# Optimization experiments

Hardware: AMD Instinct MI355X
Metric: run time of the kernel (lower is better)

The kernel has to match this reference:

```python
import jax, jax.numpy as jnp
import numpy as np

B, IN, V, H, OUT = 4096, 1024, 48, 512, 64

def setup_inputs() -> dict:
    key = jax.random.key(0)
    ks = jax.random.split(key, 6)
    s = 0.02
    x = jax.random.normal(ks[0], (B, IN), dtype=jnp.float32)
    # stacked per-vocab MLP params: hidden layers have bias, last layer bias=False
    W1 = jax.random.normal(ks[1], (V, IN, H), dtype=jnp.float32) * s
    b1 = jax.random.normal(ks[2], (V, H), dtype=jnp.float32) * s
    W2 = jax.random.normal(ks[3], (V, H, H), dtype=jnp.float32) * s
    b2 = jax.random.normal(ks[4], (V, H), dtype=jnp.float32) * s
    W3 = jax.random.normal(ks[5], (V, H, OUT), dtype=jnp.float32) * s
    return {"x": x, "W1": W1, "b1": b1, "W2": W2, "b2": b2, "W3": W3}

def reference(x, W1, b1, W2, b2, W3):
    # grouped GEMM over the vocab axis; equivalent to the per-MLP loop + cat
    h = jax.nn.relu(jnp.einsum('bi,vih->bvh', x, W1) + b1)      # [B, V, H]
    h = jax.nn.relu(jnp.einsum('bvh,vhk->bvk', h, W2) + b2)     # [B, V, H]
    o = jnp.einsum('bvk,vko->bvo', h, W3)                        # [B, V, OUT]
    # torch.cat([...], dim=-1) == reshape since outputs are in vocab order
    return o.reshape(x.shape[0], V * OUT)
```

## Files before the change

### kernel.cpp

```cpp
#include <hip/hip_runtime.h>

#define B_SZ   4096
#define IN_SZ  1024
#define V_SZ   48
#define H_SZ   512
#define OUT_SZ 64

typedef __attribute__((ext_vector_type(4))) float f32x4;
typedef __attribute__((ext_vector_type(8))) short bf16x8;
typedef __attribute__((ext_vector_type(4))) short short4v;
typedef __attribute__((ext_vector_type(4))) float float4v;

__device__ __forceinline__ short f2bf(float f){
    unsigned u = __builtin_bit_cast(unsigned, f);
    u += 0x7fffu + ((u >> 16) & 1u);
    return (short)(u >> 16);
}

__device__ __forceinline__ void gl2lds16(const void* g, void* l){
    __builtin_amdgcn_global_load_lds(
        (const __attribute__((address_space(1))) void*)g,
        (__attribute__((address_space(3))) void*)l, 16, 0, 0);
}

__global__ void k_convert_x(const float* __restrict__ x, short* __restrict__ xb){
    int i = blockIdx.x * 256 + threadIdx.x;
    float4v f = ((const float4v*)x)[i];
    short4v o = { f2bf(f.x), f2bf(f.y), f2bf(f.z), f2bf(f.w) };
    ((short4v*)xb)[i] = o;
}

__global__ __launch_bounds__(256) void k_transpose_cvt4(
    const float* __restrict__ in, short* __restrict__ out, int R, int C)
{
    __shared__ short t[64][68];
    int v  = blockIdx.z;
    int c0 = blockIdx.x * 64, r0 = blockIdx.y * 64;
    int tid = threadIdx.x;
    size_t base = (size_t)v * R * C;
    const float* inp = in + base + (size_t)r0 * C + c0;
    int g    = tid >> 4;
    int col4 = (tid & 15) * 4;
    #pragma unroll
    for (int p = 0; p < 4; ++p){
        int row = p*16 + g;
        float4v f = *(const float4v*)&inp[(size_t)row * C + col4];
        short4v s = { f2bf(f.x), f2bf(f.y), f2bf(f.z), f2bf(f.w) };
        *(short4v*)&t[row][col4] = s;
    }
    __syncthreads();
    short* outp = out + base + (size_t)c0 * R + r0;
    int r4 = (tid & 15) * 4;
    #pragma unroll
    for (int p = 0; p < 4; ++p){
        int c = p*16 + g;
        short4v s = { t[r4+0][c], t[r4+1][c], t[r4+2][c], t[r4+3][c] };
        *(short4v*)&outp[(size_t)c * R + r4] = s;
    }
}

__global__ __launch_bounds__(256) void k_gemm1(
    const short* __restrict__ xb, const short* __restrict__ W1t,
    const float* __restrict__ b1, short* __restrict__ h1)
{
    __shared__ __align__(16) short As[128*64];
    __shared__ __align__(16) short Bs[128*64];
    const int tid  = threadIdx.x;
    const int lane = tid & 63, wave = tid >> 6;
    const int l15  = lane & 15, quad = lane >> 4;
    const int wm = wave & 1, wn = wave >> 1;
    const int M0 = blockIdx.x * 128;
    const int N0 = blockIdx.y * 128;
    const int v  = blockIdx.z;

    const short* a_base = xb  + (size_t)M0 * IN_SZ;
    const short* b_base = W1t + ((size_t)v * H_SZ + N0) * IN_SZ;

    const short* asrc[4]; const short* bsrc[4]; short* adst[4]; short* bdst[4];
    #pragma unroll
    for (int j = 0; j < 4; ++j){
        int p   = j*256 + tid;
        int row = p >> 3;
        int w   = (p & 7) ^ (row & 7);
        asrc[j] = a_base + (size_t)row * IN_SZ + w*8;
        bsrc[j] = b_base + (size_t)row * IN_SZ + w*8;
        adst[j] = &As[(size_t)(j*256 + (tid & ~63)) * 8];
        bdst[j] = &Bs[(size_t)(j*256 + (tid & ~63)) * 8];
    }

    f32x4 acc[4][4];
    #pragma unroll
    for (int i = 0; i < 4; ++i)
        #pragma unroll
        for (int j = 0; j < 4; ++j) acc[i][j] = (f32x4){0.f,0.f,0.f,0.f};

    for (int k0 = 0; k0 < IN_SZ; k0 += 64){
        #pragma unroll
        for (int j = 0; j < 4; ++j){
            gl2lds16(asrc[j] + k0, adst[j]);
            gl2lds16(bsrc[j] + k0, bdst[j]);
        }
        __syncthreads();
        #pragma unroll
        for (int kk = 0; kk < 2; ++kk){
            bf16x8 a[4], b[4];
            #pragma unroll
            for (int tm = 0; tm < 4; ++tm){
                int m = wm*64 + tm*16 + l15;
                int slot = m*8 + ((kk*4 + quad) ^ (m & 7));
                a[tm] = *(const bf16x8*)&As[slot*8];
            }
            #pragma unroll
            for (int tn = 0; tn < 4; ++tn){
                int n = wn*64 + tn*16 + l15;
                int slot = n*8 + ((kk*4 + quad) ^ (n & 7));
                b[tn] = *(const bf16x8*)&Bs[slot*8];
            }
            #pragma unroll
            for (int tm = 0; tm < 4; ++tm)
                #pragma unroll
                for (int tn = 0; tn < 4; ++tn)
                    acc[tm][tn] = __builtin_amdgcn_mfma_f32_16x16x32_bf16(
                        a[tm], b[tn], acc[tm][tn], 0, 0, 0);
        }
        __syncthreads();
    }

    const float* bv = b1 + (size_t)v * H_SZ;
    short* cv = h1 + (size_t)v * (B_SZ*H_SZ);
    #pragma unroll
    for (int tn = 0; tn < 4; ++tn){
        int col = N0 + wn*64 + tn*16 + l15;
        float bb = bv[col];
        #pragma unroll
        for (int tm = 0; tm < 4; ++tm){
            int rowb = M0 + wm*64 + tm*16 + quad*4;
            #pragma unroll
            for (int r = 0; r < 4; ++r){
                float val = acc[tm][tn][r] + bb;
                val = val > 0.f ? val : 0.f;
                cv[(size_t)(rowb + r) * H_SZ + col] = f2bf(val);
            }
        }
    }
}

__global__ __launch_bounds__(512) void k_gemm23(
    const short* __restrict__ h, const short* __restrict__ W2t,
    const float* __restrict__ b2, const short* __restrict__ W3t,
    float* __restrict__ out)
{
    __shared__ __align__(16) short As[64*64];
    __shared__ __align__(16) short Bs[512*64];
    const int tid  = threadIdx.x;
    const int lane = tid & 63, wave = tid >> 6;
    const int l15  = lane & 15, quad = lane >> 4;
    const int M0 = blockIdx.x * 64;
    const int v  = blockIdx.y;

    const short* hv  = h   + (size_t)v * (B_SZ*H_SZ) + (size_t)M0 * H_SZ;
    const short* w2v = W2t + (size_t)v * (H_SZ*H_SZ);
    const short* w3v = W3t + (size_t)v * (OUT_SZ*H_SZ);

    const int rowT = tid >> 3;
    const int wT   = (tid & 7) ^ (rowT & 7);
    const short* asrc  = hv  + (size_t)rowT * H_SZ + wT*8;
    const short* bsrc0 = w2v + (size_t)rowT * H_SZ + wT*8;
    short* adst  = &As[(size_t)(tid & ~63) * 8];
    short* bdst0 = &Bs[(size_t)(tid & ~63) * 8];

    f32x4 acc[4][4];
    #pragma unroll
    for (int i = 0; i < 4; ++i)
        #pragma unroll
        for (int j = 0; j < 4; ++j) acc[i][j] = (f32x4){0.f,0.f,0.f,0.f};

    for (int k0 = 0; k0 < H_SZ; k0 += 64){
        gl2lds16(asrc + k0, adst);
        #pragma unroll
        for (int j = 0; j < 8; ++j)
            gl2lds16(bsrc0 + (size_t)j*(64*H_SZ) + k0, bdst0 + (size_t)j*512*8);
        __syncthreads();
        #pragma unroll
        for (int kk = 0; kk < 2; ++kk){
            bf16x8 a[4], b[4];
            #pragma unroll
            for (int tm = 0; tm < 4; ++tm){
                int m = tm*16 + l15;
                int slot = m*8 + ((kk*4 + quad) ^ (m & 7));
                a[tm] = *(const bf16x8*)&As[slot*8];
            }
            #pragma unroll
            for (int tn = 0; tn < 4; ++tn){
                int n = wave*64 + tn*16 + l15;
                int slot = n*8 + ((kk*4 + quad) ^ (n & 7));
                b[tn] = *(const bf16x8*)&Bs[slot*8];
            }
            #pragma unroll
            for (int tm = 0; tm < 4; ++tm)
                #pragma unroll
                for (int tn = 0; tn < 4; ++tn)
                    acc[tm][tn] = __builtin_amdgcn_mfma_f32_16x16x32_bf16(
                        a[tm], b[tn], acc[tm][tn], 0, 0, 0);
        }
        __syncthreads();
    }

    const float* bv = b2 + (size_t)v * H_SZ;
    #pragma unroll
    for (int tn = 0; tn < 4; ++tn){
        int col = wave*64 + tn*16 + l15;
        float bb = bv[col];
        int u = col >> 3, c7 = col & 7;
        #pragma unroll
        for (int tm = 0; tm < 4; ++tm){
            int rowb = tm*16 + quad*4;
            #pragma unroll
            for (int r = 0; r < 4; ++r){
                int row = rowb + r;
                float val = acc[tm][tn][r] + bb;
                val = val > 0.f ? val : 0.f;
                Bs[row*512 + ((u ^ (row & 7))*8) + c7] = f2bf(val);
            }
        }
    }
    __syncthreads();

    if (wave < 4){
        f32x4 acc3[4];
        #pragma unroll
        for (int i = 0; i < 4; ++i) acc3[i] = (f32x4){0.f,0.f,0.f,0.f};
        const int n3 = wave*16 + l15;
        const short* b3p = &w3v[(size_t)n3 * H_SZ + quad*8];
        #pragma unroll
        for (int kk = 0; kk < 16; ++kk){
            bf16x8 bfrag = *(const bf16x8*)&b3p[kk*32];
            int u = kk*4 + quad;
            #pragma unroll
            for (int tm = 0; tm < 4; ++tm){
                int m = tm*16 + l15;
                bf16x8 afrag = *(const bf16x8*)&Bs[m*512 + ((u ^ (m & 7))*8)];
                acc3[tm] = __builtin_amdgcn_mfma_f32_16x16x32_bf16(
                    afrag, bfrag, acc3[tm], 0, 0, 0);
            }
        }
        const int col = v*OUT_SZ + wave*16 + l15;
        #pragma unroll
        for (int tm = 0; tm < 4; ++tm){
            int rowb = M0 + tm*16 + quad*4;
            #pragma unroll
            for (int r = 0; r < 4; ++r)
                out[(size_t)(rowb + r) * (V_SZ*OUT_SZ) + col] = acc3[tm][r];
        }
    }
}

extern "C" void kernel_launch(void* const* d_in, const int* in_sizes, int n_in,
                              void* d_out, int out_size, void* d_ws, size_t ws_size,
                              hipStream_t stream)
{
    (void)in_sizes; (void)n_in; (void)out_size; (void)ws_size;
    const float* x  = (const float*)d_in[0];
    const float* W1 = (const float*)d_in[1];
    const float* b1 = (const float*)d_in[2];
    const float* W2 = (const float*)d_in[3];
    const float* b2 = (const float*)d_in[4];
    const float* W3 = (const float*)d_in[5];
    float* out = (float*)d_out;

    char* ws = (char*)d_ws;
    short* xb  = (short*)ws;  ws += (size_t)B_SZ * IN_SZ * 2;
    short* W1t = (short*)ws;  ws += (size_t)V_SZ * H_SZ * IN_SZ * 2;
    short* W2t = (short*)ws;  ws += (size_t)V_SZ * H_SZ * H_SZ * 2;
    short* W3t = (short*)ws;  ws += (size_t)V_SZ * OUT_SZ * H_SZ * 2;
    short* h1  = (short*)ws;

    k_convert_x<<<dim3(B_SZ*IN_SZ/1024), dim3(256), 0, stream>>>(x, xb);
    k_transpose_cvt4<<<dim3(H_SZ/64,  IN_SZ/64, V_SZ), dim3(256), 0, stream>>>(W1, W1t, IN_SZ, H_SZ);
    k_transpose_cvt4<<<dim3(H_SZ/64,  H_SZ/64,  V_SZ), dim3(256), 0, stream>>>(W2, W2t, H_SZ, H_SZ);
    k_transpose_cvt4<<<dim3(OUT_SZ/64,H_SZ/64,  V_SZ), dim3(256), 0, stream>>>(W3, W3t, H_SZ, OUT_SZ);

    k_gemm1 <<<dim3(B_SZ/128, H_SZ/128, V_SZ), dim3(256), 0, stream>>>(xb, W1t, b1, h1);
    k_gemm23<<<dim3(B_SZ/64, V_SZ), dim3(512), 0, stream>>>(h1, W2t, b2, W3t, out);
}
```

Before: 653.1 us.

## Rewrite gemm1 as 256x256 double-buffered pipelined tile with 8 waves

The first grouped GEMM moves to 256x256 output tiles per 512-thread block, with double-buffered LDS and async global-to-LDS prefetch of the next A and B tiles interleaved with MFMA phases. It adds explicit barriers, vmcnt waits and s_setprio around the MFMA bursts. The aim is to hide load latency and raise arithmetic intensity per byte loaded. In exchange it uses more registers and 128KB of LDS per block, and the hand-tuned waitcnt counts leave little margin for ordering mistakes.

```diff
diff --git a/kernel.cpp b/kernel.cpp
--- a/kernel.cpp
+++ b/kernel.cpp
@@ -22,6 +22,8 @@
         (const __attribute__((address_space(1))) void*)g,
         (__attribute__((address_space(3))) void*)l, 16, 0, 0);
 }
+
+#define MFMA_B16(d, a, b) d = __builtin_amdgcn_mfma_f32_16x16x32_bf16(a, b, d, 0, 0, 0)
 
 __global__ void k_convert_x(const float* __restrict__ x, short* __restrict__ xb){
     int i = blockIdx.x * 256 + threadIdx.x;
@@ -59,85 +61,142 @@
     }
 }
 
-__global__ __launch_bounds__(256) void k_gemm1(
+#define G1_TILE (256*64)
+#define G1_NT   (IN_SZ/64)
+
+__global__ __launch_bounds__(512) void k_gemm1(
     const short* __restrict__ xb, const short* __restrict__ W1t,
     const float* __restrict__ b1, short* __restrict__ h1)
 {
-    __shared__ __align__(16) short As[128*64];
-    __shared__ __align__(16) short Bs[128*64];
+    __shared__ __align__(16) short As[2*G1_TILE];
+    __shared__ __align__(16) short Bs[2*G1_TILE];
     const int tid  = threadIdx.x;
     const int lane = tid & 63, wave = tid >> 6;
     const int l15  = lane & 15, quad = lane >> 4;
-    const int wm = wave & 1, wn = wave >> 1;
-    const int M0 = blockIdx.x * 128;
-    const int N0 = blockIdx.y * 128;
+    const int wm = wave >> 2, wn = wave & 3;
+    const int M0 = blockIdx.x * 256;
+    const int N0 = blockIdx.y * 256;
     const int v  = blockIdx.z;
 
-    const short* a_base = xb  + (size_t)M0 * IN_SZ;
-    const short* b_base = W1t + ((size_t)v * H_SZ + N0) * IN_SZ;
-
-    const short* asrc[4]; const short* bsrc[4]; short* adst[4]; short* bdst[4];
-    #pragma unroll
-    for (int j = 0; j < 4; ++j){
-        int p   = j*256 + tid;
-        int row = p >> 3;
-        int w   = (p & 7) ^ (row & 7);
-        asrc[j] = a_base + (size_t)row * IN_SZ + w*8;
-        bsrc[j] = b_base + (size_t)row * IN_SZ + w*8;
-        adst[j] = &As[(size_t)(j*256 + (tid & ~63)) * 8];
-        bdst[j] = &Bs[(size_t)(j*256 + (tid & ~63)) * 8];
-    }
-
-    f32x4 acc[4][4];
-    #pragma unroll
-    for (int i = 0; i < 4; ++i)
+    const short* apan = xb  + (size_t)M0 * IN_SZ;
+    const short* bpan = W1t + ((size_t)v * H_SZ + N0) * IN_SZ;
+
+    const int lr    = tid >> 3;
+    const int toff  = lr * IN_SZ + (((tid & 7) ^ (lr & 7)) * 8);
+    const int wbase = tid & ~63;
+
+    auto stage = [&](const short* pan, short* lbase, int h, int j, int t){
+        gl2lds16(pan + (size_t)(h*128 + j*64) * IN_SZ + t*64 + toff,
+                 lbase + (h*1024 + j*512 + wbase) * 8);
+    };
+    auto stage_half = [&](const short* pan, short* lbase, int h, int t){
+        stage(pan, lbase, h, 0, t);
+        stage(pan, lbase, h, 1, t);
+    };
+
+    stage_half(apan, As, 0, 0); stage_half(apan, As, 1, 0);
+    stage_half(bpan, Bs, 0, 0); stage_half(bpan, Bs, 1, 0);
+    stage_half(apan, As + G1_TILE, 0, 1); stage_half(apan, As + G1_TILE, 1, 1);
+    asm volatile("s_waitcnt vmcnt(4)" ::: "memory");
+    __builtin_amdgcn_s_barrier();
+
+    f32x4 acc[8][4];
+    #pragma unroll
+    for (int i = 0; i < 8; ++i)
         #pragma unroll
         for (int j = 0; j < 4; ++j) acc[i][j] = (f32x4){0.f,0.f,0.f,0.f};
 
-    for (int k0 = 0; k0 < IN_SZ; k0 += 64){
-        #pragma unroll
-        for (int j = 0; j < 4; ++j){
-            gl2lds16(asrc[j] + k0, adst[j]);
-            gl2lds16(bsrc[j] + k0, bdst[j]);
-        }
-        __syncthreads();
-        #pragma unroll
-        for (int kk = 0; kk < 2; ++kk){
-            bf16x8 a[4], b[4];
-            #pragma unroll
-            for (int tm = 0; tm < 4; ++tm){
-                int m = wm*64 + tm*16 + l15;
-                int slot = m*8 + ((kk*4 + quad) ^ (m & 7));
-                a[tm] = *(const bf16x8*)&As[slot*8];
-            }
-            #pragma unroll
-            for (int tn = 0; tn < 4; ++tn){
-                int n = wn*64 + tn*16 + l15;
-                int slot = n*8 + ((kk*4 + quad) ^ (n & 7));
-                b[tn] = *(const bf16x8*)&Bs[slot*8];
-            }
-            #pragma unroll
-            for (int tm = 0; tm < 4; ++tm)
-                #pragma unroll
-                for (int tn = 0; tn < 4; ++tn)
-                    acc[tm][tn] = __builtin_amdgcn_mfma_f32_16x16x32_bf16(
-                        a[tm], b[tn], acc[tm][tn], 0, 0, 0);
-        }
-        __syncthreads();
+    const int x7 = l15 & 7;
+    const int abase = (wm*128 + l15) * 64;
+    const int bbase = (wn*64  + l15) * 64;
+    const int c_kk0 = ((quad)     ^ x7) * 8;
+    const int c_kk1 = ((quad + 4) ^ x7) * 8;
+
+    #pragma unroll 2
+    for (int t = 0; t < G1_NT; ++t){
+        short* Ac = As + (t & 1) * G1_TILE;
+        short* Bc = Bs + (t & 1) * G1_TILE;
+        short* Bn = Bs + ((t + 1) & 1) * G1_TILE;
+
+        bf16x8 a0[8], a1[8];
+
+        #pragma unroll
+        for (int rf = 0; rf < 8; ++rf)
+            a0[rf] = *(const bf16x8*)&Ac[abase + rf*1024 + c_kk0];
+        bf16x8 b00 = *(const bf16x8*)&Bc[bbase + 0*1024 + c_kk0];
+        bf16x8 b01 = *(const bf16x8*)&Bc[bbase + 1*1024 + c_kk0];
+        if (t + 1 < G1_NT) stage_half(bpan, Bn, 0, t + 1);
+        __builtin_amdgcn_s_barrier();
+        asm volatile("s_waitcnt lgkmcnt(0)" ::: "memory");
+        __builtin_amdgcn_s_setprio(1);
+        #pragma unroll
+        for (int rf = 0; rf < 8; ++rf){
+            MFMA_B16(acc[rf][0], a0[rf], b00);
+            MFMA_B16(acc[rf][1], a0[rf], b01);
+        }
+        __builtin_amdgcn_s_setprio(0);
+        __builtin_amdgcn_s_barrier();
+
+        #pragma unroll
+        for (int rf = 0; rf < 8; ++rf)
+            a1[rf] = *(const bf16x8*)&Ac[abase + rf*1024 + c_kk1];
+        bf16x8 b02 = *(const bf16x8*)&Bc[bbase + 2*1024 + c_kk0];
+        bf16x8 b03 = *(const bf16x8*)&Bc[bbase + 3*1024 + c_kk0];
+        if (t + 1 < G1_NT) stage_half(bpan, Bn, 1, t + 1);
+        __builtin_amdgcn_s_barrier();
+        asm volatile("s_waitcnt lgkmcnt(0)" ::: "memory");
+        __builtin_amdgcn_s_setprio(1);
+        #pragma unroll
+        for (int rf = 0; rf < 8; ++rf){
+            MFMA_B16(acc[rf][2], a0[rf], b02);
+            MFMA_B16(acc[rf][3], a0[rf], b03);
+        }
+        __builtin_amdgcn_s_setprio(0);
+        __builtin_amdgcn_s_barrier();
+
+        bf16x8 b10 = *(const bf16x8*)&Bc[bbase + 0*1024 + c_kk1];
+        bf16x8 b11 = *(const bf16x8*)&Bc[bbase + 1*1024 + c_kk1];
+        if (t + 2 < G1_NT) stage_half(apan, Ac, 0, t + 2);
+        __builtin_amdgcn_s_barrier();
+        asm volatile("s_waitcnt lgkmcnt(0)" ::: "memory");
+        __builtin_amdgcn_s_setprio(1);
+        #pragma unroll
+        for (int rf = 0; rf < 8; ++rf){
+            MFMA_B16(acc[rf][0], a1[rf], b10);
+            MFMA_B16(acc[rf][1], a1[rf], b11);
+        }
+        __builtin_amdgcn_s_setprio(0);
+        __builtin_amdgcn_s_barrier();
+
+        bf16x8 b12 = *(const bf16x8*)&Bc[bbase + 2*1024 + c_kk1];
+        bf16x8 b13 = *(const bf16x8*)&Bc[bbase + 3*1024 + c_kk1];
+        if (t + 2 < G1_NT) stage_half(apan, Ac, 1, t + 2);
+        __builtin_amdgcn_s_barrier();
+        asm volatile("s_waitcnt lgkmcnt(0)" ::: "memory");
+        __builtin_amdgcn_s_setprio(1);
+        #pragma unroll
+        for (int rf = 0; rf < 8; ++rf){
+            MFMA_B16(acc[rf][2], a1[rf], b12);
+            MFMA_B16(acc[rf][3], a1[rf], b13);
+        }
+        __builtin_amdgcn_s_setprio(0);
+        if (t + 2 < G1_NT)      { asm volatile("s_waitcnt vmcnt(4)" ::: "memory"); }
+        else if (t + 1 < G1_NT) { asm volatile("s_waitcnt vmcnt(0)" ::: "memory"); }
+        __builtin_amdgcn_s_barrier();
     }
 
     const float* bv = b1 + (size_t)v * H_SZ;
     short* cv = h1 + (size_t)v * (B_SZ*H_SZ);
     #pragma unroll
-    for (int tn = 0; tn < 4; ++tn){
-        int col = N0 + wn*64 + tn*16 + l15;
+    for (int cf = 0; cf < 4; ++cf){
+        int col = N0 + wn*64 + cf*16 + l15;
         float bb = bv[col];
         #pragma unroll
-        for (int tm = 0; tm < 4; ++tm){
-            int rowb = M0 + wm*64 + tm*16 + quad*4;
+        for (int rf = 0; rf < 8; ++rf){
+            int rowb = M0 + wm*128 + rf*16 + quad*4;
             #pragma unroll
             for (int r = 0; r < 4; ++r){
-                float val = acc[tm][tn][r] + bb;
+                float val = acc[rf][cf][r] + bb;
                 val = val > 0.f ? val : 0.f;
                 cv[(size_t)(rowb + r) * H_SZ + col] = f2bf(val);
             }
@@ -280,6 +339,6 @@
     k_transpose_cvt4<<<dim3(H_SZ/64,  H_SZ/64,  V_SZ), dim3(256), 0, stream>>>(W2, W2t, H_SZ, H_SZ);
     k_transpose_cvt4<<<dim3(OUT_SZ/64,H_SZ/64,  V_SZ), dim3(256), 0, stream>>>(W3, W3t, H_SZ, OUT_SZ);
 
-    k_gemm1 <<<dim3(B_SZ/128, H_SZ/128, V_SZ), dim3(256), 0, stream>>>(xb, W1t, b1, h1);
+    k_gemm1 <<<dim3(B_SZ/256, H_SZ/256, V_SZ), dim3(512), 0, stream>>>(xb, W1t, b1, h1);
     k_gemm23<<<dim3(B_SZ/64, V_SZ), dim3(512), 0, stream>>>(h1, W2t, b2, W3t, out);
 }
```

After: 655.8 us. Within noise of the previous version (+0.4%).

## Read W2 fragments directly from global, double-buffer A tile, split GEMM3 across all waves

Applied to the files above, without the earlier changes.

k_gemm23 no longer stages the 512x64 W2 tile in LDS each k-step. Each wave now loads its W2 B-fragments straight from global/L2 into registers. The h activation tile is double-buffered in LDS so the next tile's load overlaps the current tile's MFMAs, with setprio raised around the MFMA block. The third GEMM is spread across all 8 waves (2x4 split) instead of 4, and launch bounds request 4 blocks per CU. This trims the W2 LDS traffic and syncs, but adds uncoalesced, L2-dependent global loads on the critical path.

```diff
diff --git a/kernel.cpp b/kernel.cpp
--- a/kernel.cpp
+++ b/kernel.cpp
@@ -22,6 +22,8 @@
         (const __attribute__((address_space(1))) void*)g,
         (__attribute__((address_space(3))) void*)l, 16, 0, 0);
 }
+
+#define MFMA_B16(d, a, b) d = __builtin_amdgcn_mfma_f32_16x16x32_bf16(a, b, d, 0, 0, 0)
 
 __global__ void k_convert_x(const float* __restrict__ x, short* __restrict__ xb){
     int i = blockIdx.x * 256 + threadIdx.x;
@@ -145,13 +147,15 @@
     }
 }
 
-__global__ __launch_bounds__(512) void k_gemm23(
+__global__ __launch_bounds__(512, 4) void k_gemm23(
     const short* __restrict__ h, const short* __restrict__ W2t,
     const float* __restrict__ b2, const short* __restrict__ W3t,
     float* __restrict__ out)
 {
-    __shared__ __align__(16) short As[64*64];
-    __shared__ __align__(16) short Bs[512*64];
+    __shared__ __align__(16) short smem[2*64*64 + 64*512];
+    short* As0 = smem;
+    short* As1 = smem + 4096;
+    short* h2s = smem + 8192;
     const int tid  = threadIdx.x;
     const int lane = tid & 63, wave = tid >> 6;
     const int l15  = lane & 15, quad = lane >> 4;
@@ -164,10 +168,10 @@
 
     const int rowT = tid >> 3;
     const int wT   = (tid & 7) ^ (rowT & 7);
-    const short* asrc  = hv  + (size_t)rowT * H_SZ + wT*8;
-    const short* bsrc0 = w2v + (size_t)rowT * H_SZ + wT*8;
-    short* adst  = &As[(size_t)(tid & ~63) * 8];
-    short* bdst0 = &Bs[(size_t)(tid & ~63) * 8];
+    const short* asrc = hv + (size_t)rowT * H_SZ + wT*8;
+    const int   aoff  = (tid & ~63) * 8;
+
+    const short* b2base = w2v + (size_t)(wave*64 + l15) * H_SZ + quad*8;
 
     f32x4 acc[4][4];
     #pragma unroll
@@ -175,82 +179,91 @@
         #pragma unroll
         for (int j = 0; j < 4; ++j) acc[i][j] = (f32x4){0.f,0.f,0.f,0.f};
 
-    for (int k0 = 0; k0 < H_SZ; k0 += 64){
-        gl2lds16(asrc + k0, adst);
-        #pragma unroll
-        for (int j = 0; j < 8; ++j)
-            gl2lds16(bsrc0 + (size_t)j*(64*H_SZ) + k0, bdst0 + (size_t)j*512*8);
-        __syncthreads();
+    auto cstep = [&](const short* Acur, int t){
         #pragma unroll
         for (int kk = 0; kk < 2; ++kk){
-            bf16x8 a[4], b[4];
-            #pragma unroll
-            for (int tm = 0; tm < 4; ++tm){
-                int m = tm*16 + l15;
+            bf16x8 b[4];
+            #pragma unroll
+            for (int nf = 0; nf < 4; ++nf)
+                b[nf] = *(const bf16x8*)&b2base[nf*(16*H_SZ) + t*64 + kk*32];
+            bf16x8 a[4];
+            #pragma unroll
+            for (int mf = 0; mf < 4; ++mf){
+                int m = mf*16 + l15;
                 int slot = m*8 + ((kk*4 + quad) ^ (m & 7));
-                a[tm] = *(const bf16x8*)&As[slot*8];
-            }
-            #pragma unroll
-            for (int tn = 0; tn < 4; ++tn){
-                int n = wave*64 + tn*16 + l15;
-                int slot = n*8 + ((kk*4 + quad) ^ (n & 7));
-                b[tn] = *(const bf16x8*)&Bs[slot*8];
-            }
-            #pragma unroll
-            for (int tm = 0; tm < 4; ++tm)
+                a[mf] = *(const bf16x8*)&Acur[slot*8];
+            }
+            __builtin_amdgcn_s_setprio(1);
+            #pragma unroll
+            for (int mf = 0; mf < 4; ++mf)
                 #pragma unroll
-                for (int tn = 0; tn < 4; ++tn)
-                    acc[tm][tn] = __builtin_amdgcn_mfma_f32_16x16x32_bf16(
-                        a[tm], b[tn], acc[tm][tn], 0, 0, 0);
-        }
+                for (int nf = 0; nf < 4; ++nf)
+                    MFMA_B16(acc[mf][nf], a[mf], b[nf]);
+            __builtin_amdgcn_s_setprio(0);
+        }
+    };
+
+    gl2lds16(asrc, As0 + aoff);
+    __syncthreads();
+
+    #pragma unroll
+    for (int tp = 0; tp < 4; ++tp){
+        int t = tp*2;
+        if (t + 1 < 8) gl2lds16(asrc + (t+1)*64, As1 + aoff);
+        cstep(As0, t);
+        __syncthreads();
+        if (t + 2 < 8) gl2lds16(asrc + (t+2)*64, As0 + aoff);
+        cstep(As1, t + 1);
         __syncthreads();
     }
 
     const float* bv = b2 + (size_t)v * H_SZ;
     #pragma unroll
-    for (int tn = 0; tn < 4; ++tn){
-        int col = wave*64 + tn*16 + l15;
+    for (int nf = 0; nf < 4; ++nf){
+        int col = wave*64 + nf*16 + l15;
         float bb = bv[col];
         int u = col >> 3, c7 = col & 7;
         #pragma unroll
-        for (int tm = 0; tm < 4; ++tm){
-            int rowb = tm*16 + quad*4;
+        for (int mf = 0; mf < 4; ++mf){
+            int rowb = mf*16 + quad*4;
             #pragma unroll
             for (int r = 0; r < 4; ++r){
                 int row = rowb + r;
-                float val = acc[tm][tn][r] + bb;
+                float val = acc[mf][nf][r] + bb;
                 val = val > 0.f ? val : 0.f;
-                Bs[row*512 + ((u ^ (row & 7))*8) + c7] = f2bf(val);
+                h2s[row*512 + ((u ^ (row & 7))*8) + c7] = f2bf(val);
             }
         }
     }
     __syncthreads();
 
-    if (wave < 4){
-        f32x4 acc3[4];
-        #pragma unroll
-        for (int i = 0; i < 4; ++i) acc3[i] = (f32x4){0.f,0.f,0.f,0.f};
-        const int n3 = wave*16 + l15;
+    {
+        const int wm3 = wave >> 2;
+        const int wn3 = wave & 3;
+        f32x4 acc3[2];
+        #pragma unroll
+        for (int i = 0; i < 2; ++i) acc3[i] = (f32x4){0.f,0.f,0.f,0.f};
+        const int n3 = wn3*16 + l15;
         const short* b3p = &w3v[(size_t)n3 * H_SZ + quad*8];
         #pragma unroll
         for (int kk = 0; kk < 16; ++kk){
             bf16x8 bfrag = *(const bf16x8*)&b3p[kk*32];
             int u = kk*4 + quad;
             #pragma unroll
-            for (int tm = 0; tm < 4; ++tm){
-                int m = tm*16 + l15;
-                bf16x8 afrag = *(const bf16x8*)&Bs[m*512 + ((u ^ (m & 7))*8)];
-                acc3[tm] = __builtin_amdgcn_mfma_f32_16x16x32_bf16(
-                    afrag, bfrag, acc3[tm], 0, 0, 0);
-            }
-        }
-        const int col = v*OUT_SZ + wave*16 + l15;
-        #pragma unroll
-        for (int tm = 0; tm < 4; ++tm){
-            int rowb = M0 + tm*16 + quad*4;
+            for (int mf = 0; mf < 2; ++mf){
+                int m = wm3*32 + mf*16 + l15;
+                bf16x8 afrag = *(const bf16x8*)&h2s[m*512 + ((u ^ (m & 7))*8)];
+                acc3[mf] = __builtin_amdgcn_mfma_f32_16x16x32_bf16(
+                    afrag, bfrag, acc3[mf], 0, 0, 0);
+            }
+        }
+        const int col = v*OUT_SZ + wn3*16 + l15;
+        #pragma unroll
+        for (int mf = 0; mf < 2; ++mf){
+            int rowb = M0 + wm3*32 + mf*16 + quad*4;
             #pragma unroll
             for (int r = 0; r < 4; ++r)
-                out[(size_t)(rowb + r) * (V_SZ*OUT_SZ) + col] = acc3[tm][r];
+                out[(size_t)(rowb + r) * (V_SZ*OUT_SZ) + col] = acc3[mf][r];
         }
     }
 }
```

Result: slower. 739.7 us (+13.3%).

## Split fused layer-2/3 kernel into separate tiled GEMMs with intermediate buffer

Applied to the files above, without the earlier changes.

Adds standalone k_gemm2 (128x128 tiles, bias+ReLU, bf16 output to a new h2 workspace) and k_gemm3 (128x64 tiles writing the final output). These replace the fused k_gemm23 when the workspace is large enough. The fused kernel used a 64-row tile with a 64KB LDS weight buffer, which likely limits occupancy and reuse. The split uses smaller LDS footprints and the same swizzled layout as gemm1, but costs an extra full write and read of the [V,B,H] intermediate, plus one more launch. It falls back to the fused kernel if the workspace is too small.

```diff
diff --git a/kernel.cpp b/kernel.cpp
--- a/kernel.cpp
+++ b/kernel.cpp
@@ -145,6 +145,177 @@
     }
 }
 
+__global__ __launch_bounds__(256) void k_gemm2(
+    const short* __restrict__ h1, const short* __restrict__ W2t,
+    const float* __restrict__ b2, short* __restrict__ h2)
+{
+    __shared__ __align__(16) short As[128*64];
+    __shared__ __align__(16) short Bs[128*64];
+    const int tid  = threadIdx.x;
+    const int lane = tid & 63, wave = tid >> 6;
+    const int l15  = lane & 15, quad = lane >> 4;
+    const int wm = wave & 1, wn = wave >> 1;
+    const int M0 = blockIdx.x * 128;
+    const int N0 = blockIdx.y * 128;
+    const int v  = blockIdx.z;
+
+    const short* a_base = h1  + (size_t)v * (B_SZ*H_SZ) + (size_t)M0 * H_SZ;
+    const short* b_base = W2t + ((size_t)v * H_SZ + N0) * H_SZ;
+
+    const short* asrc[4]; const short* bsrc[4]; short* adst[4]; short* bdst[4];
+    #pragma unroll
+    for (int j = 0; j < 4; ++j){
+        int p   = j*256 + tid;
+        int row = p >> 3;
+        int w   = (p & 7) ^ (row & 7);
+        asrc[j] = a_base + (size_t)row * H_SZ + w*8;
+        bsrc[j] = b_base + (size_t)row * H_SZ + w*8;
+        adst[j] = &As[(size_t)(j*256 + (tid & ~63)) * 8];
+        bdst[j] = &Bs[(size_t)(j*256 + (tid & ~63)) * 8];
+    }
+
+    f32x4 acc[4][4];
+    #pragma unroll
+    for (int i = 0; i < 4; ++i)
+        #pragma unroll
+        for (int j = 0; j < 4; ++j) acc[i][j] = (f32x4){0.f,0.f,0.f,0.f};
+
+    for (int k0 = 0; k0 < H_SZ; k0 += 64){
+        #pragma unroll
+        for (int j = 0; j < 4; ++j){
+            gl2lds16(asrc[j] + k0, adst[j]);
+            gl2lds16(bsrc[j] + k0, bdst[j]);
+        }
+        __syncthreads();
+        #pragma unroll
+        for (int kk = 0; kk < 2; ++kk){
+            bf16x8 a[4], b[4];
+            #pragma unroll
+            for (int tm = 0; tm < 4; ++tm){
+                int m = wm*64 + tm*16 + l15;
+                int slot = m*8 + ((kk*4 + quad) ^ (m & 7));
+                a[tm] = *(const bf16x8*)&As[slot*8];
+            }
+            #pragma unroll
+            for (int tn = 0; tn < 4; ++tn){
+                int n = wn*64 + tn*16 + l15;
+                int slot = n*8 + ((kk*4 + quad) ^ (n & 7));
+                b[tn] = *(const bf16x8*)&Bs[slot*8];
+            }
+            #pragma unroll
+            for (int tm = 0; tm < 4; ++tm)
+                #pragma unroll
+                for (int tn = 0; tn < 4; ++tn)
+                    acc[tm][tn] = __builtin_amdgcn_mfma_f32_16x16x32_bf16(
+                        a[tm], b[tn], acc[tm][tn], 0, 0, 0);
+        }
+        __syncthreads();
+    }
+
+    const float* bv = b2 + (size_t)v * H_SZ;
+    short* cv = h2 + (size_t)v * (B_SZ*H_SZ);
+    #pragma unroll
+    for (int tn = 0; tn < 4; ++tn){
+        int col = N0 + wn*64 + tn*16 + l15;
+        float bb = bv[col];
+        #pragma unroll
+        for (int tm = 0; tm < 4; ++tm){
+            int rowb = M0 + wm*64 + tm*16 + quad*4;
+            #pragma unroll
+            for (int r = 0; r < 4; ++r){
+                float val = acc[tm][tn][r] + bb;
+                val = val > 0.f ? val : 0.f;
+                cv[(size_t)(rowb + r) * H_SZ + col] = f2bf(val);
+            }
+        }
+    }
+}
+
+__global__ __launch_bounds__(256) void k_gemm3(
+    const short* __restrict__ h2, const short* __restrict__ W3t,
+    float* __restrict__ out)
+{
+    __shared__ __align__(16) short As[128*64];
+    __shared__ __align__(16) short Bs[64*64];
+    const int tid  = threadIdx.x;
+    const int lane = tid & 63, wave = tid >> 6;
+    const int l15  = lane & 15, quad = lane >> 4;
+    const int wm = wave & 1, wn = wave >> 1;
+    const int M0 = blockIdx.x * 128;
+    const int v  = blockIdx.z;
+
+    const short* a_base = h2  + (size_t)v * (B_SZ*H_SZ) + (size_t)M0 * H_SZ;
+    const short* b_base = W3t + (size_t)v * (OUT_SZ*H_SZ);
+
+    const short* asrc[4]; short* adst[4];
+    #pragma unroll
+    for (int j = 0; j < 4; ++j){
+        int p   = j*256 + tid;
+        int row = p >> 3;
+        int w   = (p & 7) ^ (row & 7);
+        asrc[j] = a_base + (size_t)row * H_SZ + w*8;
+        adst[j] = &As[(size_t)(j*256 + (tid & ~63)) * 8];
+    }
+    const short* bsrc[2]; short* bdst[2];
+    #pragma unroll
+    for (int j = 0; j < 2; ++j){
+        int p   = j*256 + tid;
+        int row = p >> 3;
+        int w   = (p & 7) ^ (row & 7);
+        bsrc[j] = b_base + (size_t)row * H_SZ + w*8;
+        bdst[j] = &Bs[(size_t)(j*256 + (tid & ~63)) * 8];
+    }
+
+    f32x4 acc[4][2];
+    #pragma unroll
+    for (int i = 0; i < 4; ++i)
+        #pragma unroll
+        for (int j = 0; j < 2; ++j) acc[i][j] = (f32x4){0.f,0.f,0.f,0.f};
+
+    for (int k0 = 0; k0 < H_SZ; k0 += 64){
+        #pragma unroll
+        for (int j = 0; j < 4; ++j) gl2lds16(asrc[j] + k0, adst[j]);
+        #pragma unroll
+        for (int j = 0; j < 2; ++j) gl2lds16(bsrc[j] + k0, bdst[j]);
+        __syncthreads();
+        #pragma unroll
+        for (int kk = 0; kk < 2; ++kk){
+            bf16x8 a[4], b[2];
+            #pragma unroll
+            for (int tm = 0; tm < 4; ++tm){
+                int m = wm*64 + tm*16 + l15;
+                int slot = m*8 + ((kk*4 + quad) ^ (m & 7));
+                a[tm] = *(const bf16x8*)&As[slot*8];
+            }
+            #pragma unroll
+            for (int tn = 0; tn < 2; ++tn){
+                int n = wn*32 + tn*16 + l15;
+                int slot = n*8 + ((kk*4 + quad) ^ (n & 7));
+                b[tn] = *(const bf16x8*)&Bs[slot*8];
+            }
+            #pragma unroll
+            for (int tm = 0; tm < 4; ++tm)
+                #pragma unroll
+                for (int tn = 0; tn < 2; ++tn)
+                    acc[tm][tn] = __builtin_amdgcn_mfma_f32_16x16x32_bf16(
+                        a[tm], b[tn], acc[tm][tn], 0, 0, 0);
+        }
+        __syncthreads();
+    }
+
+    #pragma unroll
+    for (int tn = 0; tn < 2; ++tn){
+        int col = v*OUT_SZ + wn*32 + tn*16 + l15;
+        #pragma unroll
+        for (int tm = 0; tm < 4; ++tm){
+            int rowb = M0 + wm*64 + tm*16 + quad*4;
+            #pragma unroll
+            for (int r = 0; r < 4; ++r)
+                out[(size_t)(rowb + r) * (V_SZ*OUT_SZ) + col] = acc[tm][tn][r];
+        }
+    }
+}
+
 __global__ __launch_bounds__(512) void k_gemm23(
     const short* __restrict__ h, const short* __restrict__ W2t,
     const float* __restrict__ b2, const short* __restrict__ W3t,
@@ -259,7 +430,7 @@
                               void* d_out, int out_size, void* d_ws, size_t ws_size,
                               hipStream_t stream)
 {
-    (void)in_sizes; (void)n_in; (void)out_size; (void)ws_size;
+    (void)in_sizes; (void)n_in; (void)out_size;
     const float* x  = (const float*)d_in[0];
     const float* W1 = (const float*)d_in[1];
     const float* b1 = (const float*)d_in[2];
@@ -273,13 +444,21 @@
     short* W1t = (short*)ws;  ws += (size_t)V_SZ * H_SZ * IN_SZ * 2;
     short* W2t = (short*)ws;  ws += (size_t)V_SZ * H_SZ * H_SZ * 2;
     short* W3t = (short*)ws;  ws += (size_t)V_SZ * OUT_SZ * H_SZ * 2;
-    short* h1  = (short*)ws;
+    short* h1  = (short*)ws;  ws += (size_t)V_SZ * B_SZ * H_SZ * 2;
+    short* h2  = (short*)ws;  ws += (size_t)V_SZ * B_SZ * H_SZ * 2;
+    const size_t need_split = (size_t)(ws - (char*)d_ws);
 
     k_convert_x<<<dim3(B_SZ*IN_SZ/1024), dim3(256), 0, stream>>>(x, xb);
     k_transpose_cvt4<<<dim3(H_SZ/64,  IN_SZ/64, V_SZ), dim3(256), 0, stream>>>(W1, W1t, IN_SZ, H_SZ);
     k_transpose_cvt4<<<dim3(H_SZ/64,  H_SZ/64,  V_SZ), dim3(256), 0, stream>>>(W2, W2t, H_SZ, H_SZ);
     k_transpose_cvt4<<<dim3(OUT_SZ/64,H_SZ/64,  V_SZ), dim3(256), 0, stream>>>(W3, W3t, H_SZ, OUT_SZ);
 
-    k_gemm1 <<<dim3(B_SZ/128, H_SZ/128, V_SZ), dim3(256), 0, stream>>>(xb, W1t, b1, h1);
-    k_gemm23<<<dim3(B_SZ/64, V_SZ), dim3(512), 0, stream>>>(h1, W2t, b2, W3t, out);
-}
+    k_gemm1<<<dim3(B_SZ/128, H_SZ/128, V_SZ), dim3(256), 0, stream>>>(xb, W1t, b1, h1);
+
+    if (ws_size >= need_split){
+        k_gemm2<<<dim3(B_SZ/128, H_SZ/128, V_SZ), dim3(256), 0, stream>>>(h1, W2t, b2, h2);
+        k_gemm3<<<dim3(B_SZ/128, 1, V_SZ), dim3(256), 0, stream>>>(h2, W3t, out);
+    } else {
+        k_gemm23<<<dim3(B_SZ/64, V_SZ), dim3(512), 0, stream>>>(h1, W2t, b2, W3t, out);
+    }
+}
```

Result: no change. 653.3 us (+0.0%).
